# Kernel tuning notes

Hardware: AMD Instinct MI355X
Metric: run time of the kernel (lower is better)

Reference implementation:

```python
import jax, jax.numpy as jnp
import numpy as np

V, D, H, KVH, HD, I, L, T_MAX, THETA = 32000, 1024, 16, 4, 64, 2816, 2, 2048, 10000.0
EPS = 1e-5


def rmsnorm(x, w):
    return x * jax.lax.rsqrt(jnp.mean(x * x, axis=-1, keepdims=True) + EPS) * w


def rope_cos_sin(T):
    inv = 1.0 / (THETA ** (jnp.arange(0, HD, 2, dtype=jnp.float32) / HD))  # [HD/2]
    ang = jnp.arange(T, dtype=jnp.float32)[:, None] * inv[None, :]         # [T, HD/2]
    return jnp.cos(ang), jnp.sin(ang)


def apply_rope(x, cos, sin):
    # x: [B, T, h, HD]; interleaved complex pairs as in torch.view_as_complex
    x0 = x[..., 0::2]
    x1 = x[..., 1::2]
    c = cos[None, :, None, :]
    s = sin[None, :, None, :]
    o0 = x0 * c - x1 * s
    o1 = x0 * s + x1 * c
    return jnp.stack([o0, o1], axis=-1).reshape(x.shape)


def setup_inputs() -> dict:
    key = jax.random.key(0)
    ks = jax.random.split(key, 12)
    sc = 0.02
    return {
        "toks": jax.random.randint(ks[0], (1, 2048), 0, V),
        "embed": jax.random.normal(ks[1], (V, D), jnp.float32) * sc,
        "Wq": jax.random.normal(ks[2], (L, D, H * HD), jnp.float32) * sc,
        "Wk": jax.random.normal(ks[3], (L, D, KVH * HD), jnp.float32) * sc,
        "Wv": jax.random.normal(ks[4], (L, D, KVH * HD), jnp.float32) * sc,
        "Wo": jax.random.normal(ks[5], (L, H * HD, D), jnp.float32) * sc,
        "Wgate": jax.random.normal(ks[6], (L, D, I), jnp.float32) * sc,
        "Wup": jax.random.normal(ks[7], (L, D, I), jnp.float32) * sc,
        "Wdown": jax.random.normal(ks[8], (L, I, D), jnp.float32) * sc,
        "ln1_w": jnp.ones((L, D), jnp.float32),
        "ln2_w": jnp.ones((L, D), jnp.float32),
        "norm_w": jnp.ones((D,), jnp.float32),
        "Wlm": jax.random.normal(ks[9], (D, V), jnp.float32) * sc,
    }


def reference(toks, embed, Wq, Wk, Wv, Wo, Wgate, Wup, Wdown, ln1_w, ln2_w, norm_w, Wlm):
    B, T = toks.shape
    cos, sin = rope_cos_sin(T)
    causal = jnp.tril(jnp.ones((T, T), dtype=bool))
    add_mask = jnp.where(causal, 0.0, -jnp.inf).astype(jnp.float32)  # [T, T]
    n_rep = H // KVH
    scale = 1.0 / np.sqrt(HD)

    x = embed[toks]  # [B, T, D]
    for l in range(L):
        h = rmsnorm(x, ln1_w[l])
        q = (h @ Wq[l]).reshape(B, T, H, HD)
        k = (h @ Wk[l]).reshape(B, T, KVH, HD)
        v = (h @ Wv[l]).reshape(B, T, KVH, HD)
        q = apply_rope(q, cos, sin)
        k = apply_rope(k, cos, sin)
        k = jnp.repeat(k, n_rep, axis=2)  # GQA repeat_kv -> [B, T, H, HD]
        v = jnp.repeat(v, n_rep, axis=2)
        # materialized scores [B, H, T, T] (faithful to source)
        scores = jnp.einsum('bqhd,bkhd->bhqk', q, k) * scale + add_mask[None, None]
        probs = jax.nn.softmax(scores, axis=-1)
        attn = jnp.einsum('bhqk,bkhd->bqhd', probs, v).reshape(B, T, H * HD)
        x = x + attn @ Wo[l]
        h = rmsnorm(x, ln2_w[l])
        x = x + (jax.nn.silu(h @ Wgate[l]) * (h @ Wup[l])) @ Wdown[l]

    x = rmsnorm(x, norm_w)
    return x @ Wlm  # [B, T, V]
```

## Files before the change

kernel.cpp:

```cpp
#include <hip/hip_runtime.h>

#define T_SEQ 2048
#define DMODEL 1024
#define NH 16
#define NKV 4
#define HEAD_DIM 64
#define FFDIM 2816
#define NVOCAB 32000

#define QBLK 64
#define KBLK 128
#define KSS 72
#define VTS 136
#define PSS 136

using u16 = unsigned short;
typedef __bf16 bf16x8 __attribute__((ext_vector_type(8)));
typedef float f32x4 __attribute__((ext_vector_type(4)));

__device__ __forceinline__ float b2f(u16 u) {
    union { unsigned int i; float f; } v; v.i = ((unsigned int)u) << 16; return v.f;
}
__device__ __forceinline__ u16 f2b(float f) {
    unsigned int u = __builtin_bit_cast(unsigned int, f);
    unsigned int r = (u + 0x7FFFu + ((u >> 16) & 1u)) >> 16;
    return (u16)r;
}
__device__ __forceinline__ void gload16(const u16* g, u16* l) {
    __builtin_amdgcn_global_load_lds(
        (const __attribute__((address_space(1))) void*)g,
        (__attribute__((address_space(3))) void*)l, 16, 0, 0);
}

__global__ __launch_bounds__(256) void embed_kernel(const int* __restrict__ toks,
                                                    const float* __restrict__ emb,
                                                    float* __restrict__ x) {
    int idx = blockIdx.x * 256 + threadIdx.x;
    int t = idx >> 10, d = idx & 1023;
    x[idx] = emb[(size_t)toks[t] * DMODEL + d];
}

__global__ __launch_bounds__(256) void rmsnorm_kernel(const float* __restrict__ x,
                                                      const float* __restrict__ w,
                                                      u16* __restrict__ out) {
    __shared__ float red[256];
    const int row = blockIdx.x, tid = threadIdx.x;
    const float* xr = x + (size_t)row * DMODEL;
    float vals[4]; float ss = 0.f;
#pragma unroll
    for (int i = 0; i < 4; i++) { float v = xr[tid + 256 * i]; vals[i] = v; ss += v * v; }
    red[tid] = ss; __syncthreads();
    for (int s = 128; s > 0; s >>= 1) { if (tid < s) red[tid] += red[tid + s]; __syncthreads(); }
    float inv = rsqrtf(red[0] * (1.0f / DMODEL) + 1e-5f);
#pragma unroll
    for (int i = 0; i < 4; i++) {
        int c = tid + 256 * i;
        out[(size_t)row * DMODEL + c] = f2b(vals[i] * inv * w[c]);
    }
}

__global__ __launch_bounds__(256) void tcast_kernel(const float* __restrict__ in,
                                                    u16* __restrict__ out, int K, int N) {
    __shared__ float tile[32][33];
    int bx = blockIdx.x * 32;
    int by = blockIdx.y * 32;
    int tx = threadIdx.x & 31, ty = threadIdx.x >> 5;
#pragma unroll
    for (int i = 0; i < 32; i += 8)
        tile[ty + i][tx] = in[(size_t)(by + ty + i) * N + bx + tx];
    __syncthreads();
#pragma unroll
    for (int i = 0; i < 32; i += 8)
        out[(size_t)(bx + ty + i) * K + by + tx] = f2b(tile[tx][ty + i]);
}

__global__ __launch_bounds__(256) void vtcast_kernel(const u16* __restrict__ fqkv,
                                                     u16* __restrict__ vt) {
    __shared__ u16 tile[32][33];
    int bx = blockIdx.x * 32;
    int by = blockIdx.y * 32;
    int tx = threadIdx.x & 31, ty = threadIdx.x >> 5;
#pragma unroll
    for (int i = 0; i < 32; i += 8)
        tile[ty + i][tx] = fqkv[(size_t)(by + ty + i) * 1536 + 1280 + bx + tx];
    __syncthreads();
#pragma unroll
    for (int i = 0; i < 32; i += 8)
        vt[(size_t)(bx + ty + i) * T_SEQ + by + tx] = tile[tx][ty + i];
}

template<bool OUT_BF16, bool ADD>
__global__ __launch_bounds__(256) void gemm_bt_kernel(const u16* __restrict__ A,
                                                      const u16* __restrict__ BT,
                                                      void* __restrict__ Cp,
                                                      int N, int K) {
    __shared__ __align__(16) u16 As[2][128 * 32];
    __shared__ __align__(16) u16 Bs[2][128 * 32];
    const int tid = threadIdx.x;
    const int gx = gridDim.x;
    const int nwg = gx * gridDim.y;
    const int hwid = blockIdx.y * gx + blockIdx.x;
    const int q = nwg >> 3, r = nwg & 7;
    const int xcd = hwid & 7, rem = hwid >> 3;
    const int wgid = (xcd < r ? xcd * (q + 1) : r * (q + 1) + (xcd - r) * q) + rem;
    const int brow = wgid % gx, bcol = wgid / gx;

    const int w = tid >> 6, lane = tid & 63;
    const int wr = w >> 1, wc = w & 1;
    const int lg = lane >> 4, lr = lane & 15;

    f32x4 acc[4][4] = {};

    const int srow = w * 32 + (lane >> 2);
    const int scol = (lane & 3) << 3;
    const u16* gA = A + (size_t)(brow * 128 + srow) * K + scol;
    const u16* gB = BT + (size_t)(bcol * 128 + srow) * K + scol;
    const size_t koff16 = (size_t)16 * K;
    const int lofs0 = (w * 32) * 32;
    const int lofs1 = (w * 32 + 16) * 32;

    const int nt = K >> 5;
    gload16(gA, &As[0][lofs0]);
    gload16(gA + koff16, &As[0][lofs1]);
    gload16(gB, &Bs[0][lofs0]);
    gload16(gB + koff16, &Bs[0][lofs1]);
    __syncthreads();

    int cur = 0;
    for (int t = 0; t < nt; t++) {
        if (t + 1 < nt) {
            const int kb = (t + 1) << 5;
            gload16(gA + kb, &As[cur ^ 1][lofs0]);
            gload16(gA + koff16 + kb, &As[cur ^ 1][lofs1]);
            gload16(gB + kb, &Bs[cur ^ 1][lofs0]);
            gload16(gB + koff16 + kb, &Bs[cur ^ 1][lofs1]);
        }
        bf16x8 aF[4], bF[4];
#pragma unroll
        for (int m = 0; m < 4; m++)
            aF[m] = *(const bf16x8*)(&As[cur][(wr * 64 + m * 16 + lr) * 32 + lg * 8]);
#pragma unroll
        for (int n = 0; n < 4; n++)
            bF[n] = *(const bf16x8*)(&Bs[cur][(wc * 64 + n * 16 + lr) * 32 + lg * 8]);
#pragma unroll
        for (int m = 0; m < 4; m++)
#pragma unroll
            for (int n = 0; n < 4; n++)
                acc[m][n] = __builtin_amdgcn_mfma_f32_16x16x32_bf16(aF[m], bF[n], acc[m][n], 0, 0, 0);
        __syncthreads();
        cur ^= 1;
    }

#pragma unroll
    for (int m = 0; m < 4; m++)
#pragma unroll
        for (int n = 0; n < 4; n++)
#pragma unroll
            for (int j = 0; j < 4; j++) {
                int row = brow * 128 + wr * 64 + m * 16 + lg * 4 + j;
                int col = bcol * 128 + wc * 64 + n * 16 + lr;
                size_t idx = (size_t)row * N + col;
                float v = acc[m][n][j];
                if constexpr (OUT_BF16) {
                    ((u16*)Cp)[idx] = f2b(v);
                } else if constexpr (ADD) {
                    ((float*)Cp)[idx] = ((const float*)Cp)[idx] + v;
                } else {
                    ((float*)Cp)[idx] = v;
                }
            }
}

__device__ __forceinline__ int bs_off(int c, int k) {
    return c * 40 + ((((k >> 3) ^ ((c >> 3) & 3)) << 3) | (k & 7));
}

__global__ __launch_bounds__(256) void gemm_f32b_kernel(const u16* __restrict__ A,
                                                        const float* __restrict__ B,
                                                        float* __restrict__ C,
                                                        int N, int K) {
    __shared__ __align__(16) u16 As[128 * 40];
    __shared__ __align__(16) u16 Bs[128 * 40];
    const int tid = threadIdx.x;
    const int brow = blockIdx.y, bcol = blockIdx.x;
    const int wid = tid >> 6, lane = tid & 63;
    const int wr = wid >> 1, wc = wid & 1;
    const int lg = lane >> 4, lr = lane & 15;

    f32x4 acc[4][4] = {};
    const int ar = tid >> 2, ac = (tid & 3) << 3;
    const int bk = tid >> 4, bc = (tid & 15) << 3;

    for (int kb = 0; kb < K; kb += 32) {
        {
            const u16* ga = A + (size_t)(brow * 128 + ar) * K + kb + ac;
            *(uint4*)(&As[ar * 40 + ac]) = *(const uint4*)ga;
            *(uint4*)(&As[(ar + 64) * 40 + ac]) = *(const uint4*)(ga + (size_t)64 * K);
        }
        {
            const float* gb = B + (size_t)(kb + bk) * N + bcol * 128 + bc;
            float4 a0 = *(const float4*)gb;
            float4 a1 = *(const float4*)(gb + 4);
            float4 b0 = *(const float4*)(gb + (size_t)16 * N);
            float4 b1 = *(const float4*)(gb + (size_t)16 * N + 4);
            float f0[8] = {a0.x, a0.y, a0.z, a0.w, a1.x, a1.y, a1.z, a1.w};
            float f1[8] = {b0.x, b0.y, b0.z, b0.w, b1.x, b1.y, b1.z, b1.w};
#pragma unroll
            for (int i = 0; i < 8; i++) {
                Bs[bs_off(bc + i, bk)] = f2b(f0[i]);
                Bs[bs_off(bc + i, bk + 16)] = f2b(f1[i]);
            }
        }
        __syncthreads();

        bf16x8 aF[4], bF[4];
#pragma unroll
        for (int m = 0; m < 4; m++)
            aF[m] = *(const bf16x8*)(&As[(wr * 64 + m * 16 + lr) * 40 + lg * 8]);
#pragma unroll
        for (int n = 0; n < 4; n++) {
            int c = wc * 64 + n * 16 + lr;
            bF[n] = *(const bf16x8*)(&Bs[c * 40 + ((lg ^ ((c >> 3) & 3)) << 3)]);
        }
#pragma unroll
        for (int m = 0; m < 4; m++)
#pragma unroll
            for (int n = 0; n < 4; n++)
                acc[m][n] = __builtin_amdgcn_mfma_f32_16x16x32_bf16(aF[m], bF[n], acc[m][n], 0, 0, 0);
        __syncthreads();
    }

#pragma unroll
    for (int m = 0; m < 4; m++)
#pragma unroll
        for (int n = 0; n < 4; n++)
#pragma unroll
            for (int j = 0; j < 4; j++) {
                int row = brow * 128 + wr * 64 + m * 16 + lg * 4 + j;
                int col = bcol * 128 + wc * 64 + n * 16 + lr;
                C[(size_t)row * N + col] = acc[m][n][j];
            }
}

__global__ __launch_bounds__(256) void rope_kernel(const u16* __restrict__ in,
                                                   u16* __restrict__ out, int heads,
                                                   int instride, int incoloff) {
    int idx = blockIdx.x * 256 + threadIdx.x;
    int total = T_SEQ * heads * 32;
    if (idx >= total) return;
    int i = idx & 31;
    int rest = idx >> 5;
    int t = rest / heads, hh = rest - t * heads;
    float inv = expf(-(float)i * (9.210340371976184f / 32.0f));
    float ang = (float)t * inv;
    float c = cosf(ang), s = sinf(ang);
    size_t src = (size_t)t * instride + incoloff + hh * HEAD_DIM + 2 * i;
    size_t dst = (size_t)rest * HEAD_DIM + 2 * i;
    float x0 = b2f(in[src]), x1 = b2f(in[src + 1]);
    out[dst]     = f2b(x0 * c - x1 * s);
    out[dst + 1] = f2b(x0 * s + x1 * c);
}

__global__ __launch_bounds__(256) void fattn_kernel(const u16* __restrict__ q,
                                                    const u16* __restrict__ k,
                                                    const u16* __restrict__ vt,
                                                    u16* __restrict__ out) {
    __shared__ __align__(16) u16 Ks[KBLK * KSS];
    __shared__ __align__(16) u16 Vt[HEAD_DIM * VTS];
    __shared__ __align__(16) u16 Ps[QBLK * PSS];
    const int tid = threadIdx.x;
    const int qb0 = blockIdx.x * QBLK, h = blockIdx.y, kvh = h >> 2;
    const int w = tid >> 6, lane = tid & 63;
    const int lg = lane >> 4, lr = lane & 15;

    bf16x8 qf0, qf1;
    {
        const u16* src = q + ((size_t)(qb0 + w * 16 + lr) * NH + h) * HEAD_DIM;
        qf0 = *(const bf16x8*)(src + lg * 8);
        qf1 = *(const bf16x8*)(src + 32 + lg * 8);
    }

    f32x4 acc_o[4] = {};
    float m_run[4] = {-1e30f, -1e30f, -1e30f, -1e30f};
    float l_run[4] = {0.f, 0.f, 0.f, 0.f};

    const int ntiles = (qb0 + QBLK - 1) / KBLK + 1;

    for (int kt = 0; kt < ntiles; kt++) {
        const int kb = kt * KBLK;
        __syncthreads();
        for (int c = tid; c < KBLK * 8; c += 256) {
            int row = c >> 3, c8 = (c & 7) << 3;
            *(uint4*)(&Ks[row * KSS + c8]) =
                *(const uint4*)(k + ((size_t)(kb + row) * NKV + kvh) * HEAD_DIM + c8);
        }
        for (int c = tid; c < HEAD_DIM * 16; c += 256) {
            int d = c >> 4, c16 = (c & 15) << 3;
            *(uint4*)(&Vt[d * VTS + c16]) =
                *(const uint4*)(vt + (size_t)(kvh * HEAD_DIM + d) * T_SEQ + kb + c16);
        }
        __syncthreads();

        f32x4 s[8] = {};
#pragma unroll
        for (int n = 0; n < 8; n++) {
            bf16x8 kf0 = *(const bf16x8*)(&Ks[(n * 16 + lr) * KSS + lg * 8]);
            bf16x8 kf1 = *(const bf16x8*)(&Ks[(n * 16 + lr) * KSS + 32 + lg * 8]);
            s[n] = __builtin_amdgcn_mfma_f32_16x16x32_bf16(qf0, kf0, s[n], 0, 0, 0);
            s[n] = __builtin_amdgcn_mfma_f32_16x16x32_bf16(qf1, kf1, s[n], 0, 0, 0);
        }

#pragma unroll
        for (int j = 0; j < 4; j++) {
            int q_g = qb0 + w * 16 + lg * 4 + j;
            float sv[8];
            float tmax = -1e30f;
#pragma unroll
            for (int n = 0; n < 8; n++) {
                float xx = s[n][j] * 0.125f;
                if (kb + n * 16 + lr > q_g) xx = -1e30f;
                sv[n] = xx;
                tmax = fmaxf(tmax, xx);
            }
#pragma unroll
            for (int mm = 1; mm < 16; mm <<= 1) tmax = fmaxf(tmax, __shfl_xor(tmax, mm));
            float mn = fmaxf(m_run[j], tmax);
            float sc = __expf(m_run[j] - mn);
            m_run[j] = mn;
            float rsum = 0.f;
#pragma unroll
            for (int n = 0; n < 8; n++) {
                float p = __expf(sv[n] - mn);
                rsum += p;
                Ps[(w * 16 + lg * 4 + j) * PSS + n * 16 + lr] = f2b(p);
            }
#pragma unroll
            for (int mm = 1; mm < 16; mm <<= 1) rsum += __shfl_xor(rsum, mm);
            l_run[j] = l_run[j] * sc + rsum;
#pragma unroll
            for (int n = 0; n < 4; n++) acc_o[n][j] *= sc;
        }

#pragma unroll
        for (int ks = 0; ks < 4; ks++) {
            bf16x8 pf = *(const bf16x8*)(&Ps[(w * 16 + lr) * PSS + ks * 32 + lg * 8]);
#pragma unroll
            for (int n = 0; n < 4; n++) {
                bf16x8 vf = *(const bf16x8*)(&Vt[(n * 16 + lr) * VTS + ks * 32 + lg * 8]);
                acc_o[n] = __builtin_amdgcn_mfma_f32_16x16x32_bf16(pf, vf, acc_o[n], 0, 0, 0);
            }
        }
    }

#pragma unroll
    for (int n = 0; n < 4; n++)
#pragma unroll
        for (int j = 0; j < 4; j++) {
            int t = qb0 + w * 16 + lg * 4 + j;
            int d = n * 16 + lr;
            out[((size_t)t * NH + h) * HEAD_DIM + d] = f2b(acc_o[n][j] / l_run[j]);
        }
}

__global__ __launch_bounds__(256) void silu_mul_kernel(const u16* __restrict__ gu,
                                                       u16* __restrict__ out) {
    int t = blockIdx.x;
    int c = blockIdx.y * 256 + threadIdx.x;
    float gv = b2f(gu[(size_t)t * 5632 + c]);
    float uv = b2f(gu[(size_t)t * 5632 + 2816 + c]);
    float s = gv / (1.f + __expf(-gv));
    out[(size_t)t * FFDIM + c] = f2b(s * uv);
}

extern "C" void kernel_launch(void* const* d_in, const int* in_sizes, int n_in,
                              void* d_out, int out_size, void* d_ws, size_t ws_size,
                              hipStream_t stream) {
    const int*   toks = (const int*)d_in[0];
    const float* emb  = (const float*)d_in[1];
    const float* Wq   = (const float*)d_in[2];
    const float* Wk   = (const float*)d_in[3];
    const float* Wv   = (const float*)d_in[4];
    const float* Wo   = (const float*)d_in[5];
    const float* Wg   = (const float*)d_in[6];
    const float* Wu   = (const float*)d_in[7];
    const float* Wd   = (const float*)d_in[8];
    const float* ln1  = (const float*)d_in[9];
    const float* ln2  = (const float*)d_in[10];
    const float* nw   = (const float*)d_in[11];
    const float* Wlm  = (const float*)d_in[12];

    char* ob = (char*)d_out;
    const size_t MB = 1024 * 1024;
    float* x    = (float*)(ob + 0 * MB);
    u16* fqkv   = (u16*)  (ob + 8 * MB);
    u16* fGU    = (u16*)  (ob + 16 * MB);
    u16* vt     = (u16*)  (ob + 40 * MB);
    u16* qb     = (u16*)  (ob + 42 * MB);
    u16* kb     = (u16*)  (ob + 47 * MB);
    u16* attnb  = (u16*)  (ob + 48 * MB);
    u16* ffb    = (u16*)  (ob + 52 * MB);
    size_t woff = 64 * MB;
    auto walloc = [&](size_t elems) {
        u16* p = (u16*)(ob + woff);
        woff += ((elems * 2 + 255) & ~(size_t)255);
        return p;
    };
    u16 *WqkvT[2], *WoT[2], *WguT[2], *WdT[2];
    for (int l = 0; l < 2; l++) {
        WqkvT[l] = walloc((size_t)1536 * DMODEL);
        WoT[l]   = walloc((size_t)DMODEL * DMODEL);
        WguT[l]  = walloc((size_t)5632 * DMODEL);
        WdT[l]   = walloc((size_t)DMODEL * FFDIM);
    }
    u16* h = (u16*)d_ws;
    bool ws_big = ws_size >= 72 * MB;
    u16* WlmT = ws_big ? (u16*)((char*)d_ws + 4 * MB) : nullptr;
    (void)in_sizes; (void)n_in; (void)out_size;

    dim3 blk(256);
    auto tcast = [&](const float* in, u16* out, int K, int N) {
        tcast_kernel<<<dim3(N / 32, K / 32), blk, 0, stream>>>(in, out, K, N);
    };
    auto gemm_f32 = [&](const u16* A, const u16* BT, float* C, int N, int K, bool add) {
        dim3 g(T_SEQ / 128, N / 128);
        if (add) gemm_bt_kernel<false, true><<<g, blk, 0, stream>>>(A, BT, (void*)C, N, K);
        else     gemm_bt_kernel<false, false><<<g, blk, 0, stream>>>(A, BT, (void*)C, N, K);
    };
    auto gemm_b16 = [&](const u16* A, const u16* BT, u16* C, int N, int K) {
        dim3 g(T_SEQ / 128, N / 128);
        gemm_bt_kernel<true, false><<<g, blk, 0, stream>>>(A, BT, (void*)C, N, K);
    };

    for (int l = 0; l < 2; l++) {
        tcast(Wq + (size_t)l * DMODEL * NH * HEAD_DIM,  WqkvT[l],                         DMODEL, NH * HEAD_DIM);
        tcast(Wk + (size_t)l * DMODEL * NKV * HEAD_DIM, WqkvT[l] + (size_t)1024 * DMODEL, DMODEL, NKV * HEAD_DIM);
        tcast(Wv + (size_t)l * DMODEL * NKV * HEAD_DIM, WqkvT[l] + (size_t)1280 * DMODEL, DMODEL, NKV * HEAD_DIM);
        tcast(Wo + (size_t)l * DMODEL * DMODEL,         WoT[l],  DMODEL, DMODEL);
        tcast(Wg + (size_t)l * DMODEL * FFDIM,          WguT[l],                          DMODEL, FFDIM);
        tcast(Wu + (size_t)l * DMODEL * FFDIM,          WguT[l] + (size_t)FFDIM * DMODEL, DMODEL, FFDIM);
        tcast(Wd + (size_t)l * FFDIM * DMODEL,          WdT[l],  FFDIM, DMODEL);
    }
    if (WlmT) tcast(Wlm, WlmT, DMODEL, NVOCAB);

    embed_kernel<<<dim3(T_SEQ * DMODEL / 256), blk, 0, stream>>>(toks, emb, x);

    for (int l = 0; l < 2; l++) {
        rmsnorm_kernel<<<dim3(T_SEQ), blk, 0, stream>>>(x, ln1 + (size_t)l * DMODEL, h);
        gemm_b16(h, WqkvT[l], fqkv, 1536, DMODEL);
        rope_kernel<<<dim3(T_SEQ * NH * 32 / 256), blk, 0, stream>>>(fqkv, qb, NH, 1536, 0);
        rope_kernel<<<dim3(T_SEQ * NKV * 32 / 256), blk, 0, stream>>>(fqkv, kb, NKV, 1536, 1024);
        vtcast_kernel<<<dim3(8, T_SEQ / 32), blk, 0, stream>>>(fqkv, vt);
        fattn_kernel<<<dim3(T_SEQ / QBLK, NH), blk, 0, stream>>>(qb, kb, vt, attnb);
        gemm_f32(attnb, WoT[l], x, DMODEL, DMODEL, true);

        rmsnorm_kernel<<<dim3(T_SEQ), blk, 0, stream>>>(x, ln2 + (size_t)l * DMODEL, h);
        gemm_b16(h, WguT[l], fGU, 5632, DMODEL);
        silu_mul_kernel<<<dim3(T_SEQ, FFDIM / 256), blk, 0, stream>>>(fGU, ffb);
        gemm_f32(ffb, WdT[l], x, DMODEL, FFDIM, true);
    }

    rmsnorm_kernel<<<dim3(T_SEQ), blk, 0, stream>>>(x, nw, h);
    if (WlmT) {
        gemm_f32(h, WlmT, (float*)d_out, NVOCAB, DMODEL, false);
    } else {
        dim3 g(NVOCAB / 128, T_SEQ / 128);
        gemm_f32b_kernel<<<g, blk, 0, stream>>>(h, Wlm, (float*)d_out, NVOCAB, DMODEL);
    }
}
```

Before: 857.3 us.

## Add 256x256 triple-buffered MFMA GEMM for LM head projection

```diff
diff --git a/kernel.cpp b/kernel.cpp
--- a/kernel.cpp
+++ b/kernel.cpp
@@ -168,6 +168,123 @@
                 } else {
                     ((float*)Cp)[idx] = v;
                 }
+            }
+}
+
+__global__ __launch_bounds__(512) void gemm256_kernel(const u16* __restrict__ A,
+                                                      const u16* __restrict__ BT,
+                                                      float* __restrict__ C,
+                                                      int N, int K) {
+    extern __shared__ __align__(16) u16 lds[];
+    const int tid = threadIdx.x;
+    const int gx = gridDim.x;
+    const int nwg = gx * gridDim.y;
+    const int hwid = blockIdx.y * gx + blockIdx.x;
+    const int q = nwg >> 3, r = nwg & 7;
+    const int xcd = hwid & 7, rem = hwid >> 3;
+    const int wgid = (xcd < r ? xcd * (q + 1) : r * (q + 1) + (xcd - r) * q) + rem;
+    const int bR = wgid % gx, bC = wgid / gx;
+
+    const int w = tid >> 6, lane = tid & 63;
+    const int wm = w >> 2, wn = w & 3;
+    const int lg = lane >> 4, lr = lane & 15;
+
+    f32x4 acc[8][4] = {};
+
+    const int srow = lane >> 2;
+    const int scol = ((lane & 3) ^ ((lane >= 32) ? 2 : 0)) << 3;
+    const int rblk = (((lr >= 8) ? (lg ^ 2) : lg)) << 4;
+
+    const u16* Ab = A + (size_t)(bR * 256) * K + scol;
+    const u16* Bb = BT + (size_t)(bC * 256) * K + scol;
+
+    auto STAGE_A = [&](int t, int b) {
+        gload16(Ab + (size_t)(w * 16 + srow) * K + t * 32,
+                lds + (b * 16384 + w * 1024) / 2);
+        gload16(Ab + (size_t)((w + 8) * 16 + srow) * K + t * 32,
+                lds + (b * 16384 + (w + 8) * 1024) / 2);
+    };
+    auto STAGE_B = [&](int t, int b) {
+        gload16(Bb + (size_t)(w * 16 + srow) * K + t * 32,
+                lds + (49152 + b * 16384 + w * 1024) / 2);
+        gload16(Bb + (size_t)((w + 8) * 16 + srow) * K + t * 32,
+                lds + (49152 + b * 16384 + (w + 8) * 1024) / 2);
+    };
+
+    const int nt = K >> 5;
+    STAGE_A(0, 0); STAGE_B(0, 0);
+    STAGE_A(1, 1); STAGE_B(1, 1);
+    asm volatile("s_waitcnt vmcnt(4)" ::: "memory");
+    __builtin_amdgcn_s_barrier();
+
+    int cur = 0;
+    for (int t = 0; t < nt; t++) {
+        const bool st = (t + 2 < nt);
+        const int nb = (cur >= 1) ? cur - 1 : cur + 2;
+        {
+            bf16x8 aF[4], bF[4];
+#pragma unroll
+            for (int mi = 0; mi < 4; mi++)
+                aF[mi] = *(const bf16x8*)((const char*)lds + cur * 16384 +
+                                          (wm * 8 + mi) * 1024 + lr * 64 + rblk);
+#pragma unroll
+            for (int n = 0; n < 4; n++)
+                bF[n] = *(const bf16x8*)((const char*)lds + 49152 + cur * 16384 +
+                                         (wn * 4 + n) * 1024 + lr * 64 + rblk);
+            if (st) STAGE_A(t + 2, nb);
+            __builtin_amdgcn_s_barrier();
+            asm volatile("s_waitcnt lgkmcnt(0)" ::: "memory");
+            __builtin_amdgcn_sched_barrier(0);
+            __builtin_amdgcn_s_setprio(1);
+#pragma unroll
+            for (int mi = 0; mi < 4; mi++)
+#pragma unroll
+                for (int n = 0; n < 4; n++)
+                    acc[mi][n] = __builtin_amdgcn_mfma_f32_16x16x32_bf16(
+                        aF[mi], bF[n], acc[mi][n], 0, 0, 0);
+            __builtin_amdgcn_s_setprio(0);
+            __builtin_amdgcn_s_barrier();
+        }
+        {
+            bf16x8 aF[4], bF[4];
+#pragma unroll
+            for (int mi = 0; mi < 4; mi++)
+                aF[mi] = *(const bf16x8*)((const char*)lds + cur * 16384 +
+                                          (wm * 8 + 4 + mi) * 1024 + lr * 64 + rblk);
+#pragma unroll
+            for (int n = 0; n < 4; n++)
+                bF[n] = *(const bf16x8*)((const char*)lds + 49152 + cur * 16384 +
+                                         (wn * 4 + n) * 1024 + lr * 64 + rblk);
+            if (st) STAGE_B(t + 2, nb);
+            if (t + 1 < nt) {
+                if (st) asm volatile("s_waitcnt vmcnt(4)" ::: "memory");
+                else    asm volatile("s_waitcnt vmcnt(0)" ::: "memory");
+            }
+            __builtin_amdgcn_s_barrier();
+            asm volatile("s_waitcnt lgkmcnt(0)" ::: "memory");
+            __builtin_amdgcn_sched_barrier(0);
+            __builtin_amdgcn_s_setprio(1);
+#pragma unroll
+            for (int mi = 0; mi < 4; mi++)
+#pragma unroll
+                for (int n = 0; n < 4; n++)
+                    acc[4 + mi][n] = __builtin_amdgcn_mfma_f32_16x16x32_bf16(
+                        aF[mi], bF[n], acc[4 + mi][n], 0, 0, 0);
+            __builtin_amdgcn_s_setprio(0);
+            __builtin_amdgcn_s_barrier();
+        }
+        cur = (cur == 2) ? 0 : cur + 1;
+    }
+
+#pragma unroll
+    for (int m = 0; m < 8; m++)
+#pragma unroll
+        for (int n = 0; n < 4; n++)
+#pragma unroll
+            for (int jj = 0; jj < 4; jj++) {
+                int row = bR * 256 + wm * 128 + m * 16 + lg * 4 + jj;
+                int col = bC * 256 + wn * 64 + n * 16 + lr;
+                C[(size_t)row * N + col] = acc[m][n][jj];
             }
 }
 
@@ -461,7 +578,11 @@
 
     rmsnorm_kernel<<<dim3(T_SEQ), blk, 0, stream>>>(x, nw, h);
     if (WlmT) {
-        gemm_f32(h, WlmT, (float*)d_out, NVOCAB, DMODEL, false);
+        (void)hipFuncSetAttribute(reinterpret_cast<const void*>(gemm256_kernel),
+                                  hipFuncAttributeMaxDynamicSharedMemorySize, 98304);
+        dim3 g(T_SEQ / 256, NVOCAB / 256);
+        gemm256_kernel<<<g, dim3(512), 98304, stream>>>(h, WlmT, (float*)d_out,
+                                                        NVOCAB, DMODEL);
     } else {
         dim3 g(NVOCAB / 128, T_SEQ / 128);
         gemm_f32b_kernel<<<g, blk, 0, stream>>>(h, Wlm, (float*)d_out, NVOCAB, DMODEL);
```

Measured after the change: 842.3 us. Within noise of the previous version (-1.8%).
